# Optimization experiments

Hardware: AMD Instinct MI355X
Metric: run time of the kernel (lower is better)

Reference implementation:

```python
import jax, jax.numpy as jnp
import numpy as np


def setup_inputs() -> dict:
    key = jax.random.key(0)
    x = jax.random.normal(key, (8, 64, 64, 64), dtype=jnp.float32)  # [B,C,H,W]
    return {"x": x}


def reference(x):
    B, C, H, W = x.shape
    N = H * W
    x1 = x.reshape(B, C, N)                 # [B,C,N]
    x2 = jnp.swapaxes(x1, 1, 2)             # [B,N,C]
    # unscaled self-attention scores over spatial positions
    attn = jnp.einsum('bnc,bcm->bnm', x2, x1)   # [B,N,N]
    attn = jax.nn.softmax(attn, axis=-1)
    y = jnp.einsum('bnm,bmc->bnc', attn, x2)    # [B,N,C]
    y = jnp.swapaxes(y, 1, 2).reshape(B, C, H, W)
    return (y, attn)
```

## Files before the change

kernel.cpp:

```cpp
#include <hip/hip_runtime.h>
#include <math.h>

#define BATCH 8
#define CD 64
#define ND 4096
#define MR 128

typedef short bf16x8 __attribute__((ext_vector_type(8)));
typedef float f32x4 __attribute__((ext_vector_type(4)));

static __device__ __forceinline__ unsigned short f2bf(float f) {
    unsigned int u = __float_as_uint(f);
    u += 0x7fff + ((u >> 16) & 1);
    return (unsigned short)(u >> 16);
}
static __device__ __forceinline__ float bf2f(unsigned short h) {
    return __uint_as_float(((unsigned int)h) << 16);
}

__global__ __launch_bounds__(256) void convert_kernel(const float* __restrict__ x,
        unsigned short* __restrict__ xt_hi, unsigned short* __restrict__ xt_lo,
        unsigned short* __restrict__ xcm_hi) {
    __shared__ unsigned short Thi[64][68];
    __shared__ unsigned short Tlo[64][68];
    const int b = blockIdx.y, n0 = blockIdx.x * 64, t = threadIdx.x;
    const float* xb = x + (size_t)b * CD * ND;

    for (int r = 0; r < 4; ++r) {
        int f4 = t + r * 256;
        int c  = f4 >> 4;
        int nc = (f4 & 15) * 4;
        float4 v = *(const float4*)&xb[(size_t)c * ND + n0 + nc];
        float vv[4] = {v.x, v.y, v.z, v.w};
        unsigned short h[4];
        unsigned long long packed = 0;
        for (int j = 0; j < 4; ++j) {
            h[j] = f2bf(vv[j]);
            unsigned short lo = f2bf(vv[j] - bf2f(h[j]));
            Thi[c][nc + j] = h[j];
            Tlo[c][nc + j] = lo;
            packed |= ((unsigned long long)h[j]) << (16 * j);
        }
        *(unsigned long long*)&xcm_hi[((size_t)b * CD + c) * ND + n0 + nc] = packed;
    }
    __syncthreads();

    const int n = t >> 2, c0 = (t & 3) * 16;
    unsigned short hb[16], lb[16];
    for (int j = 0; j < 16; ++j) { hb[j] = Thi[c0 + j][n]; lb[j] = Tlo[c0 + j][n]; }
    size_t base = ((size_t)b * ND + n0 + n) * CD + c0;
    *(uint4*)&xt_hi[base]     = *(uint4*)&hb[0];
    *(uint4*)&xt_hi[base + 8] = *(uint4*)&hb[8];
    *(uint4*)&xt_lo[base]     = *(uint4*)&lb[0];
    *(uint4*)&xt_lo[base + 8] = *(uint4*)&lb[8];
}

__global__ __launch_bounds__(256, 1) void attn_kernel(
        const unsigned short* __restrict__ xt_hi,
        const unsigned short* __restrict__ xt_lo,
        const unsigned short* __restrict__ xcm_hi,
        float* __restrict__ y, float* __restrict__ attn) {
    extern __shared__ char smem[];
    unsigned short (*Ahi)[72] = (unsigned short(*)[72])(smem);
    unsigned short (*Alo)[72] = (unsigned short(*)[72])(smem + 18432);
    unsigned short (*Bhi)[72] = (unsigned short(*)[72])(smem + 36864);
    unsigned short (*Blo)[72] = (unsigned short(*)[72])(smem + 46080);
    unsigned short (*Xpv)[72] = (unsigned short(*)[72])(smem + 55296);
    unsigned short (*Ppv)[72] = (unsigned short(*)[72])(smem + 64512);

    const int t  = threadIdx.x;
    const int w  = t >> 6;
    const int l  = t & 63;
    const int q  = l >> 4;
    const int lc = l & 15;
    const int b  = blockIdx.y;
    const int n0 = blockIdx.x * MR;

    const unsigned short* xthi_b = xt_hi + (size_t)b * ND * CD;
    const unsigned short* xtlo_b = xt_lo + (size_t)b * ND * CD;
    const unsigned short* xcm_b  = xcm_hi + (size_t)b * CD * ND;
    float* attn_b = attn + (size_t)b * ND * ND;

    for (int r = 0; r < 4; ++r) {
        int u = t + r * 256;
        int row = u >> 3;
        int k8  = (u & 7) * 8;
        *(uint4*)&Ahi[row][k8] = *(const uint4*)&xthi_b[(size_t)(n0 + row) * CD + k8];
        *(uint4*)&Alo[row][k8] = *(const uint4*)&xtlo_b[(size_t)(n0 + row) * CD + k8];
    }

    float runmax[2][4], runsum[2][4];
    #pragma unroll
    for (int rt = 0; rt < 2; ++rt)
        #pragma unroll
        for (int i = 0; i < 4; ++i) { runmax[rt][i] = -INFINITY; runsum[rt][i] = 0.f; }

    for (int m0 = 0; m0 < ND; m0 += 64) {
        __syncthreads();
        for (int r = 0; r < 2; ++r) {
            int u = t * 2 + r;
            int row = u >> 3;
            int k8  = (u & 7) * 8;
            *(uint4*)&Bhi[row][k8] = *(const uint4*)&xthi_b[(size_t)(m0 + row) * CD + k8];
            *(uint4*)&Blo[row][k8] = *(const uint4*)&xtlo_b[(size_t)(m0 + row) * CD + k8];
        }
        __syncthreads();

        bf16x8 ah[2][2], al[2][2];
        #pragma unroll
        for (int rt = 0; rt < 2; ++rt)
            #pragma unroll
            for (int ks = 0; ks < 2; ++ks) {
                int row = w * 32 + rt * 16 + lc;
                ah[rt][ks] = *(const bf16x8*)(const void*)&Ahi[row][ks * 32 + q * 8];
                al[rt][ks] = *(const bf16x8*)(const void*)&Alo[row][ks * 32 + q * 8];
            }
        f32x4 accs[2][4];
        #pragma unroll
        for (int ct = 0; ct < 4; ++ct) {
            bf16x8 bh[2], bl[2];
            #pragma unroll
            for (int ks = 0; ks < 2; ++ks) {
                bh[ks] = *(const bf16x8*)(const void*)&Bhi[ct * 16 + lc][ks * 32 + q * 8];
                bl[ks] = *(const bf16x8*)(const void*)&Blo[ct * 16 + lc][ks * 32 + q * 8];
            }
            #pragma unroll
            for (int rt = 0; rt < 2; ++rt) {
                f32x4 acc = {0.f, 0.f, 0.f, 0.f};
                #pragma unroll
                for (int ks = 0; ks < 2; ++ks) {
                    acc = __builtin_amdgcn_mfma_f32_16x16x32_bf16(ah[rt][ks], bh[ks], acc, 0, 0, 0);
                    acc = __builtin_amdgcn_mfma_f32_16x16x32_bf16(ah[rt][ks], bl[ks], acc, 0, 0, 0);
                    acc = __builtin_amdgcn_mfma_f32_16x16x32_bf16(al[rt][ks], bh[ks], acc, 0, 0, 0);
                }
                accs[rt][ct] = acc;
            }
        }
        #pragma unroll
        for (int rt = 0; rt < 2; ++rt)
            #pragma unroll
            for (int i = 0; i < 4; ++i) {
                float v0 = accs[rt][0][i], v1 = accs[rt][1][i];
                float v2 = accs[rt][2][i], v3 = accs[rt][3][i];
                float lm = fmaxf(fmaxf(v0, v1), fmaxf(v2, v3));
                float M  = fmaxf(runmax[rt][i], lm);
                float s  = __expf(v0 - M) + __expf(v1 - M) + __expf(v2 - M) + __expf(v3 - M);
                runsum[rt][i] = runsum[rt][i] * __expf(runmax[rt][i] - M) + s;
                runmax[rt][i] = M;
            }
    }

    #pragma unroll
    for (int rt = 0; rt < 2; ++rt)
        #pragma unroll
        for (int i = 0; i < 4; ++i) {
            float M = runmax[rt][i], S = runsum[rt][i];
            #pragma unroll
            for (int off = 1; off < 16; off <<= 1) {
                float M2 = __shfl_xor(M, off);
                float S2 = __shfl_xor(S, off);
                float Mn = fmaxf(M, M2);
                S = S * __expf(M - Mn) + S2 * __expf(M2 - Mn);
                M = Mn;
            }
            runmax[rt][i] = M;
            runsum[rt][i] = 1.0f / S;
        }

    f32x4 pvacc[2][4];
    #pragma unroll
    for (int rt = 0; rt < 2; ++rt)
        #pragma unroll
        for (int ct = 0; ct < 4; ++ct) { f32x4 z = {0.f,0.f,0.f,0.f}; pvacc[rt][ct] = z; }

    for (int m0 = 0; m0 < ND; m0 += 64) {
        __syncthreads();
        for (int r = 0; r < 2; ++r) {
            int u = t * 2 + r;
            int row = u >> 3;
            int k8  = (u & 7) * 8;
            *(uint4*)&Bhi[row][k8] = *(const uint4*)&xthi_b[(size_t)(m0 + row) * CD + k8];
            *(uint4*)&Blo[row][k8] = *(const uint4*)&xtlo_b[(size_t)(m0 + row) * CD + k8];
            *(uint4*)&Xpv[row][k8] = *(const uint4*)&xcm_b[(size_t)row * ND + m0 + k8];
        }
        __syncthreads();

        bf16x8 ah[2][2], al[2][2];
        #pragma unroll
        for (int rt = 0; rt < 2; ++rt)
            #pragma unroll
            for (int ks = 0; ks < 2; ++ks) {
                int row = w * 32 + rt * 16 + lc;
                ah[rt][ks] = *(const bf16x8*)(const void*)&Ahi[row][ks * 32 + q * 8];
                al[rt][ks] = *(const bf16x8*)(const void*)&Alo[row][ks * 32 + q * 8];
            }
        f32x4 accs[2][4];
        #pragma unroll
        for (int ct = 0; ct < 4; ++ct) {
            bf16x8 bh[2], bl[2];
            #pragma unroll
            for (int ks = 0; ks < 2; ++ks) {
                bh[ks] = *(const bf16x8*)(const void*)&Bhi[ct * 16 + lc][ks * 32 + q * 8];
                bl[ks] = *(const bf16x8*)(const void*)&Blo[ct * 16 + lc][ks * 32 + q * 8];
            }
            #pragma unroll
            for (int rt = 0; rt < 2; ++rt) {
                f32x4 acc = {0.f, 0.f, 0.f, 0.f};
                #pragma unroll
                for (int ks = 0; ks < 2; ++ks) {
                    acc = __builtin_amdgcn_mfma_f32_16x16x32_bf16(ah[rt][ks], bh[ks], acc, 0, 0, 0);
                    acc = __builtin_amdgcn_mfma_f32_16x16x32_bf16(ah[rt][ks], bl[ks], acc, 0, 0, 0);
                    acc = __builtin_amdgcn_mfma_f32_16x16x32_bf16(al[rt][ks], bh[ks], acc, 0, 0, 0);
                }
                accs[rt][ct] = acc;
            }
        }

        #pragma unroll
        for (int rt = 0; rt < 2; ++rt)
            #pragma unroll
            for (int ct = 0; ct < 4; ++ct)
                #pragma unroll
                for (int i = 0; i < 4; ++i) {
                    float p = __expf(accs[rt][ct][i] - runmax[rt][i]) * runsum[rt][i];
                    int rloc = w * 32 + rt * 16 + q * 4 + i;
                    __builtin_nontemporal_store(p,
                        &attn_b[(size_t)(n0 + rloc) * ND + m0 + ct * 16 + lc]);
                    Ppv[rloc][ct * 16 + lc] = f2bf(p);
                }
        __asm__ volatile("s_waitcnt lgkmcnt(0)" ::: "memory");

        #pragma unroll
        for (int rt = 0; rt < 2; ++rt)
            #pragma unroll
            for (int ks = 0; ks < 2; ++ks) {
                bf16x8 pa = *(const bf16x8*)(const void*)&Ppv[w * 32 + rt * 16 + lc][ks * 32 + q * 8];
                #pragma unroll
                for (int ct = 0; ct < 4; ++ct) {
                    bf16x8 xv = *(const bf16x8*)(const void*)&Xpv[ct * 16 + lc][ks * 32 + q * 8];
                    pvacc[rt][ct] = __builtin_amdgcn_mfma_f32_16x16x32_bf16(pa, xv, pvacc[rt][ct], 0, 0, 0);
                }
            }
    }

    #pragma unroll
    for (int rt = 0; rt < 2; ++rt)
        #pragma unroll
        for (int ct = 0; ct < 4; ++ct) {
            int c = ct * 16 + lc;
            int n = n0 + w * 32 + rt * 16 + q * 4;
            float4 v = make_float4(pvacc[rt][ct][0], pvacc[rt][ct][1],
                                   pvacc[rt][ct][2], pvacc[rt][ct][3]);
            *(float4*)&y[((size_t)b * CD + c) * ND + n] = v;
        }
}

extern "C" void kernel_launch(void* const* d_in, const int* in_sizes, int n_in,
                              void* d_out, int out_size, void* d_ws, size_t ws_size,
                              hipStream_t stream) {
    const float* x = (const float*)d_in[0];
    float* y    = (float*)d_out;
    float* attn = (float*)d_out + (size_t)BATCH * CD * ND;

    unsigned short* xt_hi  = (unsigned short*)d_ws;
    unsigned short* xt_lo  = xt_hi + (size_t)BATCH * ND * CD;
    unsigned short* xcm_hi = xt_lo + (size_t)BATCH * ND * CD;

    hipFuncSetAttribute(reinterpret_cast<const void*>(attn_kernel),
                        hipFuncAttributeMaxDynamicSharedMemorySize, 82944);

    convert_kernel<<<dim3(ND / 64, BATCH), 256, 0, stream>>>(x, xt_hi, xt_lo, xcm_hi);
    attn_kernel<<<dim3(ND / MR, BATCH), 256, 82944, stream>>>(xt_hi, xt_lo, xcm_hi, y, attn);
}
```

Baseline: 712.4 us.

## Use precomputed row norms as softmax max, double-buffer tiles, smaller row blocks

```diff
diff --git a/kernel.cpp b/kernel.cpp
--- a/kernel.cpp
+++ b/kernel.cpp
@@ -4,7 +4,7 @@
 #define BATCH 8
 #define CD 64
 #define ND 4096
-#define MR 128
+#define MR 64
 
 typedef short bf16x8 __attribute__((ext_vector_type(8)));
 typedef float f32x4 __attribute__((ext_vector_type(4)));
@@ -20,7 +20,7 @@
 
 __global__ __launch_bounds__(256) void convert_kernel(const float* __restrict__ x,
         unsigned short* __restrict__ xt_hi, unsigned short* __restrict__ xt_lo,
-        unsigned short* __restrict__ xcm_hi) {
+        unsigned short* __restrict__ xcm_hi, float* __restrict__ norms) {
     __shared__ unsigned short Thi[64][68];
     __shared__ unsigned short Tlo[64][68];
     const int b = blockIdx.y, n0 = blockIdx.x * 64, t = threadIdx.x;
@@ -32,14 +32,13 @@
         int nc = (f4 & 15) * 4;
         float4 v = *(const float4*)&xb[(size_t)c * ND + n0 + nc];
         float vv[4] = {v.x, v.y, v.z, v.w};
-        unsigned short h[4];
         unsigned long long packed = 0;
         for (int j = 0; j < 4; ++j) {
-            h[j] = f2bf(vv[j]);
-            unsigned short lo = f2bf(vv[j] - bf2f(h[j]));
-            Thi[c][nc + j] = h[j];
+            unsigned short hi = f2bf(vv[j]);
+            unsigned short lo = f2bf(vv[j] - bf2f(hi));
+            Thi[c][nc + j] = hi;
             Tlo[c][nc + j] = lo;
-            packed |= ((unsigned long long)h[j]) << (16 * j);
+            packed |= ((unsigned long long)hi) << (16 * j);
         }
         *(unsigned long long*)&xcm_hi[((size_t)b * CD + c) * ND + n0 + nc] = packed;
     }
@@ -47,212 +46,185 @@
 
     const int n = t >> 2, c0 = (t & 3) * 16;
     unsigned short hb[16], lb[16];
-    for (int j = 0; j < 16; ++j) { hb[j] = Thi[c0 + j][n]; lb[j] = Tlo[c0 + j][n]; }
+    float nrm = 0.f;
+    #pragma unroll
+    for (int j = 0; j < 16; ++j) {
+        hb[j] = Thi[c0 + j][n];
+        lb[j] = Tlo[c0 + j][n];
+        float xv = bf2f(hb[j]) + bf2f(lb[j]);
+        nrm = fmaf(xv, xv, nrm);
+    }
     size_t base = ((size_t)b * ND + n0 + n) * CD + c0;
     *(uint4*)&xt_hi[base]     = *(uint4*)&hb[0];
     *(uint4*)&xt_hi[base + 8] = *(uint4*)&hb[8];
     *(uint4*)&xt_lo[base]     = *(uint4*)&lb[0];
     *(uint4*)&xt_lo[base + 8] = *(uint4*)&lb[8];
-}
-
-__global__ __launch_bounds__(256, 1) void attn_kernel(
+
+    nrm += __shfl_xor(nrm, 1);
+    nrm += __shfl_xor(nrm, 2);
+    if ((t & 3) == 0) norms[(size_t)b * ND + n0 + n] = nrm;
+}
+
+__global__ __launch_bounds__(256, 2) void attn_kernel(
         const unsigned short* __restrict__ xt_hi,
         const unsigned short* __restrict__ xt_lo,
         const unsigned short* __restrict__ xcm_hi,
+        const float* __restrict__ norms,
         float* __restrict__ y, float* __restrict__ attn) {
-    extern __shared__ char smem[];
-    unsigned short (*Ahi)[72] = (unsigned short(*)[72])(smem);
-    unsigned short (*Alo)[72] = (unsigned short(*)[72])(smem + 18432);
-    unsigned short (*Bhi)[72] = (unsigned short(*)[72])(smem + 36864);
-    unsigned short (*Blo)[72] = (unsigned short(*)[72])(smem + 46080);
-    unsigned short (*Xpv)[72] = (unsigned short(*)[72])(smem + 55296);
-    unsigned short (*Ppv)[72] = (unsigned short(*)[72])(smem + 64512);
+    __shared__ unsigned short Bhi[2][64][72];
+    __shared__ unsigned short Blo[2][64][72];
+    __shared__ unsigned short Xpv[2][64][72];
+    __shared__ unsigned short Ppv[64][72];
 
     const int t  = threadIdx.x;
     const int w  = t >> 6;
     const int l  = t & 63;
     const int q  = l >> 4;
     const int lc = l & 15;
-    const int b  = blockIdx.y;
-    const int n0 = blockIdx.x * MR;
+
+    const int lin = blockIdx.x + gridDim.x * blockIdx.y;
+    const int swz = (lin & 7) * 64 + (lin >> 3);
+    const int b  = swz >> 6;
+    const int n0 = (swz & 63) * MR;
 
     const unsigned short* xthi_b = xt_hi + (size_t)b * ND * CD;
     const unsigned short* xtlo_b = xt_lo + (size_t)b * ND * CD;
     const unsigned short* xcm_b  = xcm_hi + (size_t)b * CD * ND;
+    const float* norms_b = norms + (size_t)b * ND;
     float* attn_b = attn + (size_t)b * ND * ND;
 
-    for (int r = 0; r < 4; ++r) {
-        int u = t + r * 256;
-        int row = u >> 3;
-        int k8  = (u & 7) * 8;
-        *(uint4*)&Ahi[row][k8] = *(const uint4*)&xthi_b[(size_t)(n0 + row) * CD + k8];
-        *(uint4*)&Alo[row][k8] = *(const uint4*)&xtlo_b[(size_t)(n0 + row) * CD + k8];
-    }
-
-    float runmax[2][4], runsum[2][4];
-    #pragma unroll
-    for (int rt = 0; rt < 2; ++rt)
-        #pragma unroll
-        for (int i = 0; i < 4; ++i) { runmax[rt][i] = -INFINITY; runsum[rt][i] = 0.f; }
-
-    for (int m0 = 0; m0 < ND; m0 += 64) {
-        __syncthreads();
-        for (int r = 0; r < 2; ++r) {
-            int u = t * 2 + r;
-            int row = u >> 3;
-            int k8  = (u & 7) * 8;
-            *(uint4*)&Bhi[row][k8] = *(const uint4*)&xthi_b[(size_t)(m0 + row) * CD + k8];
-            *(uint4*)&Blo[row][k8] = *(const uint4*)&xtlo_b[(size_t)(m0 + row) * CD + k8];
-        }
-        __syncthreads();
-
-        bf16x8 ah[2][2], al[2][2];
-        #pragma unroll
-        for (int rt = 0; rt < 2; ++rt)
-            #pragma unroll
-            for (int ks = 0; ks < 2; ++ks) {
-                int row = w * 32 + rt * 16 + lc;
-                ah[rt][ks] = *(const bf16x8*)(const void*)&Ahi[row][ks * 32 + q * 8];
-                al[rt][ks] = *(const bf16x8*)(const void*)&Alo[row][ks * 32 + q * 8];
-            }
-        f32x4 accs[2][4];
+    const size_t arow = (size_t)(n0 + w * 16 + lc) * CD;
+    const bf16x8 ah0 = *(const bf16x8*)(const void*)&xthi_b[arow + q * 8];
+    const bf16x8 ah1 = *(const bf16x8*)(const void*)&xthi_b[arow + 32 + q * 8];
+    const bf16x8 al0 = *(const bf16x8*)(const void*)&xtlo_b[arow + q * 8];
+    const bf16x8 al1 = *(const bf16x8*)(const void*)&xtlo_b[arow + 32 + q * 8];
+
+    const float4 Mv = *(const float4*)&norms_b[n0 + w * 16 + q * 4];
+    const float M[4] = {Mv.x, Mv.y, Mv.z, Mv.w};
+
+    const int srow = t >> 2;
+    const int skk  = (t & 3) * 16;
+
+    uint4 ph0, ph1, pl0, pl1, px0, px1;
+    auto loadB = [&](int m0) {
+        const size_t rb = (size_t)(m0 + srow) * CD + skk;
+        ph0 = *(const uint4*)&xthi_b[rb];
+        ph1 = *(const uint4*)&xthi_b[rb + 8];
+        pl0 = *(const uint4*)&xtlo_b[rb];
+        pl1 = *(const uint4*)&xtlo_b[rb + 8];
+    };
+    auto writeB = [&](int buf) {
+        *(uint4*)&Bhi[buf][srow][skk]     = ph0;
+        *(uint4*)&Bhi[buf][srow][skk + 8] = ph1;
+        *(uint4*)&Blo[buf][srow][skk]     = pl0;
+        *(uint4*)&Blo[buf][srow][skk + 8] = pl1;
+    };
+    auto loadX = [&](int m0) {
+        const size_t rx = (size_t)srow * ND + m0 + skk;
+        px0 = *(const uint4*)&xcm_b[rx];
+        px1 = *(const uint4*)&xcm_b[rx + 8];
+    };
+    auto writeX = [&](int buf) {
+        *(uint4*)&Xpv[buf][srow][skk]     = px0;
+        *(uint4*)&Xpv[buf][srow][skk + 8] = px1;
+    };
+
+    auto computeS = [&](int cb, int ct) -> f32x4 {
+        const unsigned short* bhp = &Bhi[cb][ct * 16 + lc][q * 8];
+        const unsigned short* blp = &Blo[cb][ct * 16 + lc][q * 8];
+        bf16x8 bh0 = *(const bf16x8*)(const void*)bhp;
+        bf16x8 bh1 = *(const bf16x8*)(const void*)(bhp + 32);
+        bf16x8 bl0 = *(const bf16x8*)(const void*)blp;
+        bf16x8 bl1 = *(const bf16x8*)(const void*)(blp + 32);
+        f32x4 a0 = {0.f, 0.f, 0.f, 0.f}, a1 = {0.f, 0.f, 0.f, 0.f};
+        a0 = __builtin_amdgcn_mfma_f32_16x16x32_bf16(ah0, bh0, a0, 0, 0, 0);
+        a1 = __builtin_amdgcn_mfma_f32_16x16x32_bf16(ah1, bh1, a1, 0, 0, 0);
+        a0 = __builtin_amdgcn_mfma_f32_16x16x32_bf16(ah0, bl0, a0, 0, 0, 0);
+        a1 = __builtin_amdgcn_mfma_f32_16x16x32_bf16(ah1, bl1, a1, 0, 0, 0);
+        a0 = __builtin_amdgcn_mfma_f32_16x16x32_bf16(al0, bh0, a0, 0, 0, 0);
+        a1 = __builtin_amdgcn_mfma_f32_16x16x32_bf16(al1, bh1, a1, 0, 0, 0);
+        return a0 + a1;
+    };
+
+    float ssum[4] = {0.f, 0.f, 0.f, 0.f};
+    loadB(0);
+    writeB(0);
+    __syncthreads();
+    int cur = 0;
+    for (int it = 0; it < ND / 64; ++it) {
+        loadB(((it + 1) & 63) * 64);
         #pragma unroll
         for (int ct = 0; ct < 4; ++ct) {
-            bf16x8 bh[2], bl[2];
+            f32x4 s = computeS(cur, ct);
             #pragma unroll
-            for (int ks = 0; ks < 2; ++ks) {
-                bh[ks] = *(const bf16x8*)(const void*)&Bhi[ct * 16 + lc][ks * 32 + q * 8];
-                bl[ks] = *(const bf16x8*)(const void*)&Blo[ct * 16 + lc][ks * 32 + q * 8];
-            }
-            #pragma unroll
-            for (int rt = 0; rt < 2; ++rt) {
-                f32x4 acc = {0.f, 0.f, 0.f, 0.f};
-                #pragma unroll
-                for (int ks = 0; ks < 2; ++ks) {
-                    acc = __builtin_amdgcn_mfma_f32_16x16x32_bf16(ah[rt][ks], bh[ks], acc, 0, 0, 0);
-                    acc = __builtin_amdgcn_mfma_f32_16x16x32_bf16(ah[rt][ks], bl[ks], acc, 0, 0, 0);
-                    acc = __builtin_amdgcn_mfma_f32_16x16x32_bf16(al[rt][ks], bh[ks], acc, 0, 0, 0);
-                }
-                accs[rt][ct] = acc;
-            }
-        }
+            for (int i = 0; i < 4; ++i) ssum[i] += __expf(s[i] - M[i]);
+        }
+        writeB(cur ^ 1);
+        cur ^= 1;
+        __syncthreads();
+    }
+
+    float inv[4];
+    #pragma unroll
+    for (int i = 0; i < 4; ++i) {
+        float s = ssum[i];
+        s += __shfl_xor(s, 1);
+        s += __shfl_xor(s, 2);
+        s += __shfl_xor(s, 4);
+        s += __shfl_xor(s, 8);
+        inv[i] = 1.0f / s;
+    }
+
+    f32x4 pvacc[4];
+    #pragma unroll
+    for (int ct = 0; ct < 4; ++ct) { f32x4 z = {0.f, 0.f, 0.f, 0.f}; pvacc[ct] = z; }
+
+    loadX(0);
+    writeX(0);
+    __syncthreads();
+    cur = 0;
+    for (int it = 0; it < ND / 64; ++it) {
+        const int m0 = it * 64;
+        const int mn = ((it + 1) & 63) * 64;
+        loadB(mn);
+        loadX(mn);
+
         #pragma unroll
-        for (int rt = 0; rt < 2; ++rt)
+        for (int ct = 0; ct < 4; ++ct) {
+            f32x4 s = computeS(cur, ct);
             #pragma unroll
             for (int i = 0; i < 4; ++i) {
-                float v0 = accs[rt][0][i], v1 = accs[rt][1][i];
-                float v2 = accs[rt][2][i], v3 = accs[rt][3][i];
-                float lm = fmaxf(fmaxf(v0, v1), fmaxf(v2, v3));
-                float M  = fmaxf(runmax[rt][i], lm);
-                float s  = __expf(v0 - M) + __expf(v1 - M) + __expf(v2 - M) + __expf(v3 - M);
-                runsum[rt][i] = runsum[rt][i] * __expf(runmax[rt][i] - M) + s;
-                runmax[rt][i] = M;
+                float p = __expf(s[i] - M[i]) * inv[i];
+                __builtin_nontemporal_store(p,
+                    &attn_b[(size_t)(n0 + w * 16 + q * 4 + i) * ND + m0 + ct * 16 + lc]);
+                Ppv[w * 16 + q * 4 + i][ct * 16 + lc] = f2bf(p);
             }
-    }
-
-    #pragma unroll
-    for (int rt = 0; rt < 2; ++rt)
+        }
+        __asm__ volatile("s_waitcnt lgkmcnt(0)" ::: "memory");
+
         #pragma unroll
-        for (int i = 0; i < 4; ++i) {
-            float M = runmax[rt][i], S = runsum[rt][i];
+        for (int ks = 0; ks < 2; ++ks) {
+            bf16x8 pa = *(const bf16x8*)(const void*)&Ppv[w * 16 + lc][ks * 32 + q * 8];
             #pragma unroll
-            for (int off = 1; off < 16; off <<= 1) {
-                float M2 = __shfl_xor(M, off);
-                float S2 = __shfl_xor(S, off);
-                float Mn = fmaxf(M, M2);
-                S = S * __expf(M - Mn) + S2 * __expf(M2 - Mn);
-                M = Mn;
+            for (int ct = 0; ct < 4; ++ct) {
+                bf16x8 xv = *(const bf16x8*)(const void*)&Xpv[cur][ct * 16 + lc][ks * 32 + q * 8];
+                pvacc[ct] = __builtin_amdgcn_mfma_f32_16x16x32_bf16(pa, xv, pvacc[ct], 0, 0, 0);
             }
-            runmax[rt][i] = M;
-            runsum[rt][i] = 1.0f / S;
-        }
-
-    f32x4 pvacc[2][4];
-    #pragma unroll
-    for (int rt = 0; rt < 2; ++rt)
-        #pragma unroll
-        for (int ct = 0; ct < 4; ++ct) { f32x4 z = {0.f,0.f,0.f,0.f}; pvacc[rt][ct] = z; }
-
-    for (int m0 = 0; m0 < ND; m0 += 64) {
+        }
+
+        writeB(cur ^ 1);
+        writeX(cur ^ 1);
+        cur ^= 1;
         __syncthreads();
-        for (int r = 0; r < 2; ++r) {
-            int u = t * 2 + r;
-            int row = u >> 3;
-            int k8  = (u & 7) * 8;
-            *(uint4*)&Bhi[row][k8] = *(const uint4*)&xthi_b[(size_t)(m0 + row) * CD + k8];
-            *(uint4*)&Blo[row][k8] = *(const uint4*)&xtlo_b[(size_t)(m0 + row) * CD + k8];
-            *(uint4*)&Xpv[row][k8] = *(const uint4*)&xcm_b[(size_t)row * ND + m0 + k8];
-        }
-        __syncthreads();
-
-        bf16x8 ah[2][2], al[2][2];
-        #pragma unroll
-        for (int rt = 0; rt < 2; ++rt)
-            #pragma unroll
-            for (int ks = 0; ks < 2; ++ks) {
-                int row = w * 32 + rt * 16 + lc;
-                ah[rt][ks] = *(const bf16x8*)(const void*)&Ahi[row][ks * 32 + q * 8];
-                al[rt][ks] = *(const bf16x8*)(const void*)&Alo[row][ks * 32 + q * 8];
-            }
-        f32x4 accs[2][4];
-        #pragma unroll
-        for (int ct = 0; ct < 4; ++ct) {
-            bf16x8 bh[2], bl[2];
-            #pragma unroll
-            for (int ks = 0; ks < 2; ++ks) {
-                bh[ks] = *(const bf16x8*)(const void*)&Bhi[ct * 16 + lc][ks * 32 + q * 8];
-                bl[ks] = *(const bf16x8*)(const void*)&Blo[ct * 16 + lc][ks * 32 + q * 8];
-            }
-            #pragma unroll
-            for (int rt = 0; rt < 2; ++rt) {
-                f32x4 acc = {0.f, 0.f, 0.f, 0.f};
-                #pragma unroll
-                for (int ks = 0; ks < 2; ++ks) {
-                    acc = __builtin_amdgcn_mfma_f32_16x16x32_bf16(ah[rt][ks], bh[ks], acc, 0, 0, 0);
-                    acc = __builtin_amdgcn_mfma_f32_16x16x32_bf16(ah[rt][ks], bl[ks], acc, 0, 0, 0);
-                    acc = __builtin_amdgcn_mfma_f32_16x16x32_bf16(al[rt][ks], bh[ks], acc, 0, 0, 0);
-                }
-                accs[rt][ct] = acc;
-            }
-        }
-
-        #pragma unroll
-        for (int rt = 0; rt < 2; ++rt)
-            #pragma unroll
-            for (int ct = 0; ct < 4; ++ct)
-                #pragma unroll
-                for (int i = 0; i < 4; ++i) {
-                    float p = __expf(accs[rt][ct][i] - runmax[rt][i]) * runsum[rt][i];
-                    int rloc = w * 32 + rt * 16 + q * 4 + i;
-                    __builtin_nontemporal_store(p,
-                        &attn_b[(size_t)(n0 + rloc) * ND + m0 + ct * 16 + lc]);
-                    Ppv[rloc][ct * 16 + lc] = f2bf(p);
-                }
-        __asm__ volatile("s_waitcnt lgkmcnt(0)" ::: "memory");
-
-        #pragma unroll
-        for (int rt = 0; rt < 2; ++rt)
-            #pragma unroll
-            for (int ks = 0; ks < 2; ++ks) {
-                bf16x8 pa = *(const bf16x8*)(const void*)&Ppv[w * 32 + rt * 16 + lc][ks * 32 + q * 8];
-                #pragma unroll
-                for (int ct = 0; ct < 4; ++ct) {
-                    bf16x8 xv = *(const bf16x8*)(const void*)&Xpv[ct * 16 + lc][ks * 32 + q * 8];
-                    pvacc[rt][ct] = __builtin_amdgcn_mfma_f32_16x16x32_bf16(pa, xv, pvacc[rt][ct], 0, 0, 0);
-                }
-            }
-    }
-
-    #pragma unroll
-    for (int rt = 0; rt < 2; ++rt)
-        #pragma unroll
-        for (int ct = 0; ct < 4; ++ct) {
-            int c = ct * 16 + lc;
-            int n = n0 + w * 32 + rt * 16 + q * 4;
-            float4 v = make_float4(pvacc[rt][ct][0], pvacc[rt][ct][1],
-                                   pvacc[rt][ct][2], pvacc[rt][ct][3]);
-            *(float4*)&y[((size_t)b * CD + c) * ND + n] = v;
-        }
+    }
+
+    #pragma unroll
+    for (int ct = 0; ct < 4; ++ct) {
+        int c = ct * 16 + lc;
+        int n = n0 + w * 16 + q * 4;
+        float4 v = make_float4(pvacc[ct][0], pvacc[ct][1], pvacc[ct][2], pvacc[ct][3]);
+        *(float4*)&y[((size_t)b * CD + c) * ND + n] = v;
+    }
 }
 
 extern "C" void kernel_launch(void* const* d_in, const int* in_sizes, int n_in,
@@ -265,10 +237,8 @@
     unsigned short* xt_hi  = (unsigned short*)d_ws;
     unsigned short* xt_lo  = xt_hi + (size_t)BATCH * ND * CD;
     unsigned short* xcm_hi = xt_lo + (size_t)BATCH * ND * CD;
-
-    hipFuncSetAttribute(reinterpret_cast<const void*>(attn_kernel),
-                        hipFuncAttributeMaxDynamicSharedMemorySize, 82944);
-
-    convert_kernel<<<dim3(ND / 64, BATCH), 256, 0, stream>>>(x, xt_hi, xt_lo, xcm_hi);
-    attn_kernel<<<dim3(ND / MR, BATCH), 256, 82944, stream>>>(xt_hi, xt_lo, xcm_hi, y, attn);
-}
+    float* norms = (float*)(xcm_hi + (size_t)BATCH * CD * ND);
+
+    convert_kernel<<<dim3(ND / 64, BATCH), 256, 0, stream>>>(x, xt_hi, xt_lo, xcm_hi, norms);
+    attn_kernel<<<dim3(ND / MR, BATCH), 256, 0, stream>>>(xt_hi, xt_lo, xcm_hi, norms, y, attn);
+}
```

New measurement: 626.7 us. -12.0%, faster.
